# Optimization experiments

Measured on AMD Instinct MI355X. Metric: run time of the kernel, lower is better.

The kernel has to match this reference:

```python
import jax, jax.numpy as jnp
import numpy as np

OUT = 260        # RESIZE_OUTPUT_IMAGES_SHAPE
TH = 0.8         # OD_SCORE_TH
PCT = 1.0        # INTERNAL_PERCENTAGE_IMAGE_TOTAKE
N_BOXES = 10     # loop bound in original call()
TAPS = 6         # lanczos3 support (radius 3 -> 6 taps, antialias=False)


def _lanczos_taps(src, size):
    """src: (OUT,) float sample coords in crop-local space; size: traced int crop size.
    Returns clamped tap indices (OUT,6) and normalized lanczos3 weights (OUT,6)."""
    base = jnp.floor(src).astype(jnp.int32) - 2
    taps = base[:, None] + jnp.arange(TAPS, dtype=jnp.int32)          # (OUT,6)
    d = src[:, None] - taps.astype(src.dtype)
    w = jnp.where(jnp.abs(d) < 3.0, jnp.sinc(d) * jnp.sinc(d / 3.0), 0.0)
    w = w / jnp.sum(w, axis=1, keepdims=True)
    idx = jnp.clip(taps, 0, size - 1)
    return idx, w


def _crop_resize(img, box):
    """img: (H,W,3). box: (4,) normalized [ymin,xmin,ymax,xmax] -> (OUT,OUT,3).
    Matches tf.image.resize lanczos3 (antialias=False): half-pixel centers, clamped edges."""
    H, W = img.shape[0], img.shape[1]
    y0 = (box[0] * H).astype(jnp.int32)
    x0 = (box[1] * W).astype(jnp.int32)
    y1 = (box[2] * H).astype(jnp.int32)
    x1 = (box[3] * W).astype(jnp.int32)
    ch = jnp.maximum(y1 - y0, 1)
    cw = jnp.maximum(x1 - x0, 1)
    o = jnp.arange(OUT, dtype=img.dtype)
    src_h = (o + 0.5) * (ch.astype(img.dtype) / OUT) - 0.5
    src_w = (o + 0.5) * (cw.astype(img.dtype) / OUT) - 0.5
    idx_h, w_h = _lanczos_taps(src_h, ch)
    idx_w, w_w = _lanczos_taps(src_w, cw)
    idx_h = idx_h + y0
    idx_w = idx_w + x0
    # vertical pass: gather 6 row taps per output row, reduce -> (OUT, W, 3)
    rows = jnp.einsum('pa,pawc->pwc', w_h, img[idx_h])
    # horizontal pass: gather 6 col taps per output col, reduce -> (OUT, OUT, 3)
    out = jnp.einsum('qb,pqbc->pqc', w_w, rows[:, idx_w])
    return out


def setup_inputs() -> dict:
    key = jax.random.key(0)
    k1, k2, k3, k4 = jax.random.split(key, 4)
    # scores: first 10 mostly above threshold, rest below
    s_hi = 0.85 + 0.15 * jax.random.uniform(k1, (N_BOXES,), dtype=jnp.float32)
    s_lo = 0.8 * jax.random.uniform(k2, (100 - N_BOXES,), dtype=jnp.float32)
    od_scores = jnp.concatenate([s_hi, s_lo])
    # bboxes (ymin,xmin,ymax,xmax) with guaranteed positive crop sizes
    u = jax.random.uniform(k3, (100, 4), dtype=jnp.float32)
    od_bboxes = jnp.stack([u[:, 0] * 0.45, u[:, 1] * 0.45,
                           0.55 + 0.45 * u[:, 2], 0.55 + 0.45 * u[:, 3]], axis=1)
    image = jax.random.normal(k4, (1, 2048, 2048, 3), dtype=jnp.float32)
    return {"od_scores": od_scores, "od_bboxes": od_bboxes, "image": image}


def reference(od_scores, od_bboxes, image):
    img = image[0]                           # (H,W,3)
    b10 = od_bboxes[:N_BOXES]
    s10 = od_scores[:N_BOXES]
    valid = ((od_scores[0] >= TH) & (s10 >= TH)
             & (b10[:, 1] >= 0.5 - PCT / 2.0)
             & (b10[:, 3] <= 0.5 + PCT / 2.0))
    crops = jax.vmap(lambda b: _crop_resize(img, b))(b10)   # (10,OUT,OUT,3)
    return crops * valid[:, None, None, None].astype(img.dtype)
```

## Files before the change

### kernel.cpp

```cpp
#include <hip/hip_runtime.h>
#include <math.h>

#define OUT 260
#define TAPS 6
#define IMG_H 2048
#define IMG_W 2048
#define ROW_F (IMG_W * 3)
#define NB 10
#define TH 0.8f
#define SEGS 9
#define QB 32
#define LROW 800
#define MAXM 14

__device__ __forceinline__ float sincf(float x) {
    if (x == 0.0f) return 1.0f;
    float px = 3.14159265358979323846f * x;
    return __sinf(px) / px;
}


__global__ __launch_bounds__(320) void tables_kernel(
    const float* __restrict__ scores, const float* __restrict__ boxes,
    float* __restrict__ htab, float* __restrict__ vtab)
{
    const int box = blockIdx.x;
    const float b0 = boxes[box * 4 + 0];
    const float b1 = boxes[box * 4 + 1];
    const float b2 = boxes[box * 4 + 2];
    const float b3 = boxes[box * 4 + 3];

    const int y0 = (int)(b0 * (float)IMG_H);
    const int x0 = (int)(b1 * (float)IMG_W);
    const int y1 = (int)(b2 * (float)IMG_H);
    const int x1 = (int)(b3 * (float)IMG_W);
    const int ch = max(y1 - y0, 1);
    const int cw = max(x1 - x0, 1);

    const bool valid = (scores[0] >= TH) && (scores[box] >= TH)
                    && (b1 >= 0.0f) && (b3 <= 1.0f);
    const float vmask = valid ? 1.0f : 0.0f;

    const int t = threadIdx.x;
    if (t >= OUT) return;

    {
        const float src = ((float)t + 0.5f) * ((float)cw / (float)OUT) - 0.5f;
        const int base = (int)floorf(src) - 2;
        float w[TAPS]; int id[TAPS];
        float s = 0.0f;
        #pragma unroll
        for (int k = 0; k < TAPS; ++k) {
            const float d = src - (float)(base + k);
            const float wv = (fabsf(d) < 3.0f) ? sincf(d) * sincf(d * (1.0f / 3.0f)) : 0.0f;
            w[k] = wv; s += wv;
            int tt = base + k; tt = tt < 0 ? 0 : tt; tt = tt > cw - 1 ? cw - 1 : tt;
            id[k] = (x0 + tt) * 3;
        }
        const float inv = 1.0f / s;
        float* h = htab + ((size_t)(box * OUT + t) << 4);
        int*   hi = (int*)h;
        #pragma unroll
        for (int k = 0; k < TAPS; ++k) { h[k] = w[k] * inv; hi[8 + k] = id[k]; }
        h[6] = 0.0f; h[7] = 0.0f; hi[14] = 0; hi[15] = 0;
    }

    {
        const float src = ((float)t + 0.5f) * ((float)ch / (float)OUT) - 0.5f;
        const int base = (int)floorf(src) - 2;
        float w[TAPS]; int id[TAPS];
        float s = 0.0f;
        #pragma unroll
        for (int k = 0; k < TAPS; ++k) {
            const float d = src - (float)(base + k);
            const float wv = (fabsf(d) < 3.0f) ? sincf(d) * sincf(d * (1.0f / 3.0f)) : 0.0f;
            w[k] = wv; s += wv;
            int tt = base + k; tt = tt < 0 ? 0 : tt; tt = tt > ch - 1 ? ch - 1 : tt;
            id[k] = tt + y0;
        }
        const float inv = vmask / s;
        float* v = vtab + ((size_t)(box * OUT + t) << 4);
        int*   vi = (int*)v;
        #pragma unroll
        for (int k = 0; k < TAPS; ++k) { v[k] = w[k] * inv; vi[8 + k] = id[k]; }
        v[6] = 0.0f; v[7] = 0.0f; vi[14] = base; vi[15] = 0;
    }
}

__global__ __launch_bounds__(64) void crop_resize_pair(
    const float* __restrict__ img,
    const float* __restrict__ htab,
    const float* __restrict__ vtab,
    float* __restrict__ out)
{
    const int seg = blockIdx.x;
    const int py  = blockIdx.y;
    const int box = blockIdx.z;
    const int q0  = seg * QB;
    const int qcount = min(QB, OUT - q0);
    const int p0 = 2 * py;

    const float* v0 = vtab + ((size_t)(box * OUT + p0) << 4);
    const float* v1 = vtab + ((size_t)(box * OUT + p0 + 1) << 4);
    const int* vi0 = (const int*)v0;
    const int* vi1 = (const int*)v1;

    int dlt = vi1[14] - vi0[14];
    dlt = dlt < 0 ? 0 : (dlt > MAXM - TAPS ? MAXM - TAPS : dlt);
    const int m = dlt + TAPS;

    float wa[MAXM], wb[MAXM];
    int   rowi[MAXM];
    #pragma unroll
    for (int j = 0; j < MAXM; ++j) {
        const float wA = (j < TAPS) ? v0[j] : 0.0f;
        const int jb = j - dlt;
        const float wB = (jb >= 0 && jb < TAPS) ? v1[jb] : 0.0f;
        wa[j] = wA; wb[j] = wB;
        rowi[j] = (j < TAPS) ? vi0[8 + j] : vi1[8 + ((jb < 0) ? 0 : (jb > 5 ? 5 : jb))];
    }

    const int* hi_first = (const int*)(htab + ((size_t)(box * OUT + q0) << 4));
    const int* hi_last  = (const int*)(htab + ((size_t)(box * OUT + q0 + qcount - 1) << 4));
    const int start_f = hi_first[8] & ~3;
    const int n_f     = ((hi_last[13] + 3) - start_f + 3) & ~3;

    __shared__ float lds[2 * LROW];

    for (int f = threadIdx.x * 4; f < n_f; f += 64 * 4) {
        float4 a0 = make_float4(0.f, 0.f, 0.f, 0.f);
        float4 a1 = make_float4(0.f, 0.f, 0.f, 0.f);
        #pragma unroll
        for (int j = 0; j < TAPS; ++j) {
            const float4 v = *(const float4*)(img + (size_t)rowi[j] * ROW_F + start_f + f);
            a0.x = fmaf(wa[j], v.x, a0.x); a0.y = fmaf(wa[j], v.y, a0.y);
            a0.z = fmaf(wa[j], v.z, a0.z); a0.w = fmaf(wa[j], v.w, a0.w);
            a1.x = fmaf(wb[j], v.x, a1.x); a1.y = fmaf(wb[j], v.y, a1.y);
            a1.z = fmaf(wb[j], v.z, a1.z); a1.w = fmaf(wb[j], v.w, a1.w);
        }
        for (int j = TAPS; j < m; ++j) {
            const float4 v = *(const float4*)(img + (size_t)rowi[j] * ROW_F + start_f + f);
            a1.x = fmaf(wb[j], v.x, a1.x); a1.y = fmaf(wb[j], v.y, a1.y);
            a1.z = fmaf(wb[j], v.z, a1.z); a1.w = fmaf(wb[j], v.w, a1.w);
        }
        *(float4*)(lds + f) = a0;
        *(float4*)(lds + LROW + f) = a1;
    }
    __syncthreads();

    const int t    = threadIdx.x;
    const int sel  = t >> 5;
    const int qi   = t & 31;
    if (qi < qcount) {
        const int q = q0 + qi;
        const float* h  = htab + ((size_t)(box * OUT + q) << 4);
        const int*   hi = (const int*)h;
        const float* l  = lds + sel * LROW;
        float a0 = 0.0f, a1 = 0.0f, a2 = 0.0f;
        #pragma unroll
        for (int k = 0; k < TAPS; ++k) {
            const float w  = h[k];
            const int   li = hi[8 + k] - start_f;
            a0 = fmaf(w, l[li + 0], a0);
            a1 = fmaf(w, l[li + 1], a1);
            a2 = fmaf(w, l[li + 2], a2);
        }
        const size_t o = (((size_t)box * OUT + (p0 + sel)) * OUT + q) * 3;
        out[o + 0] = a0;
        out[o + 1] = a1;
        out[o + 2] = a2;
    }
}

__global__ __launch_bounds__(256) void crop_resize_fallback(
    const float* __restrict__ scores, const float* __restrict__ boxes,
    const float* __restrict__ img, float* __restrict__ out)
{
    const int p = blockIdx.x, box = blockIdx.y;
    const float b0 = boxes[box*4+0], b1 = boxes[box*4+1];
    const float b2 = boxes[box*4+2], b3 = boxes[box*4+3];
    const int y0 = (int)(b0*(float)IMG_H), x0 = (int)(b1*(float)IMG_W);
    const int y1 = (int)(b2*(float)IMG_H), x1 = (int)(b3*(float)IMG_W);
    const int ch = max(y1-y0,1), cw = max(x1-x0,1);
    const bool valid = (scores[0]>=TH)&&(scores[box]>=TH)&&(b1>=0.0f)&&(b3<=1.0f);
    const float vmask = valid?1.0f:0.0f;
    float wh[TAPS]; int ih[TAPS];
    {
        const float src = ((float)p+0.5f)*((float)ch/(float)OUT)-0.5f;
        const int base = (int)floorf(src)-2;
        float s = 0.0f;
        #pragma unroll
        for (int a = 0; a < TAPS; ++a) {
            const float d = src-(float)(base+a);
            const float w = (fabsf(d)<3.0f)?sincf(d)*sincf(d*(1.0f/3.0f)):0.0f;
            wh[a]=w; s+=w;
            int t=base+a; t=t<0?0:t; t=t>ch-1?ch-1:t; ih[a]=t+y0;
        }
        const float inv = 1.0f/s;
        #pragma unroll
        for (int a = 0; a < TAPS; ++a) wh[a]*=inv;
    }
    const int start_f = (x0*3)&~3;
    const int end_f = (x0+cw)*3;
    const int n_f = end_f-start_f;
    __shared__ float lds[6152];
    {
        const float* r0 = img+(size_t)ih[0]*ROW_F+start_f;
        const float* r1 = img+(size_t)ih[1]*ROW_F+start_f;
        const float* r2 = img+(size_t)ih[2]*ROW_F+start_f;
        const float* r3 = img+(size_t)ih[3]*ROW_F+start_f;
        const float* r4 = img+(size_t)ih[4]*ROW_F+start_f;
        const float* r5 = img+(size_t)ih[5]*ROW_F+start_f;
        for (int f = threadIdx.x*4; f < n_f; f += 256*4) {
            const float4 u0=*(const float4*)(r0+f), u1=*(const float4*)(r1+f);
            const float4 u2=*(const float4*)(r2+f), u3=*(const float4*)(r3+f);
            const float4 u4=*(const float4*)(r4+f), u5=*(const float4*)(r5+f);
            float4 acc;
            acc.x=wh[0]*u0.x+wh[1]*u1.x+wh[2]*u2.x+wh[3]*u3.x+wh[4]*u4.x+wh[5]*u5.x;
            acc.y=wh[0]*u0.y+wh[1]*u1.y+wh[2]*u2.y+wh[3]*u3.y+wh[4]*u4.y+wh[5]*u5.y;
            acc.z=wh[0]*u0.z+wh[1]*u1.z+wh[2]*u2.z+wh[3]*u3.z+wh[4]*u4.z+wh[5]*u5.z;
            acc.w=wh[0]*u0.w+wh[1]*u1.w+wh[2]*u2.w+wh[3]*u3.w+wh[4]*u4.w+wh[5]*u5.w;
            *(float4*)(lds+f)=acc;
        }
    }
    __syncthreads();
    const float wscale = (float)cw/(float)OUT;
    for (int q = threadIdx.x; q < OUT; q += 256) {
        const float src = ((float)q+0.5f)*wscale-0.5f;
        const int basew = (int)floorf(src)-2;
        float ww[TAPS]; float s = 0.0f;
        #pragma unroll
        for (int k = 0; k < TAPS; ++k) {
            const float d = src-(float)(basew+k);
            const float w = (fabsf(d)<3.0f)?sincf(d)*sincf(d*(1.0f/3.0f)):0.0f;
            ww[k]=w; s+=w;
        }
        const float inv = 1.0f/s;
        float a0=0,a1=0,a2=0;
        #pragma unroll
        for (int k = 0; k < TAPS; ++k) {
            int t=basew+k; t=t<0?0:t; t=t>cw-1?cw-1:t;
            const int hb=(x0+t)*3-start_f;
            a0=fmaf(ww[k],lds[hb+0],a0);
            a1=fmaf(ww[k],lds[hb+1],a1);
            a2=fmaf(ww[k],lds[hb+2],a2);
        }
        const float mfac = vmask*inv;
        const size_t o = (((size_t)box*OUT+p)*OUT+q)*3;
        out[o+0]=a0*mfac; out[o+1]=a1*mfac; out[o+2]=a2*mfac;
    }
}

extern "C" void kernel_launch(void* const* d_in, const int* in_sizes, int n_in,
                              void* d_out, int out_size, void* d_ws, size_t ws_size,
                              hipStream_t stream) {
    const float* scores = (const float*)d_in[0];
    const float* boxes  = (const float*)d_in[1];
    const float* img    = (const float*)d_in[2];
    float* out = (float*)d_out;

    const size_t tab_bytes = (size_t)NB * OUT * 16 * sizeof(float);
    if (ws_size < 2 * tab_bytes) {
        crop_resize_fallback<<<dim3(OUT, NB), dim3(256), 0, stream>>>(scores, boxes, img, out);
        return;
    }
    float* htab = (float*)d_ws;
    float* vtab = (float*)((char*)d_ws + tab_bytes);

    tables_kernel<<<dim3(NB), dim3(320), 0, stream>>>(scores, boxes, htab, vtab);
    crop_resize_pair<<<dim3(SEGS, OUT / 2, NB), dim3(64), 0, stream>>>(img, htab, vtab, out);
}
```

Before: 119.2 us.

## Compute four output rows per block sharing a union of image row loads

Replaces the two-rows-per-block vertical pass with a block that handles a group of four output rows, loading the union of their source image rows once and accumulating into four register accumulators per float4 column chunk. Column segments widen to 48 outputs, so fewer blocks re-read overlapping image columns, and the per-row weight/index tables are staged in shared memory. This cuts redundant global reads of image rows at the cost of many more accumulator registers (80 floats) and a larger LDS footprint, which may lower occupancy, and fewer total blocks.

```diff
diff --git a/kernel.cpp b/kernel.cpp
--- a/kernel.cpp
+++ b/kernel.cpp
@@ -8,10 +8,12 @@
 #define ROW_F (IMG_W * 3)
 #define NB 10
 #define TH 0.8f
-#define SEGS 9
-#define QB 32
-#define LROW 800
-#define MAXM 14
+#define SEGS 6
+#define QB 48
+#define G 4
+#define LROW 1152
+#define MAXM 32
+#define NF 5
 
 __device__ __forceinline__ float sincf(float x) {
     if (x == 0.0f) return 1.0f;
@@ -87,37 +89,63 @@
     }
 }
 
-__global__ __launch_bounds__(64) void crop_resize_pair(
+__global__ __launch_bounds__(64) void crop_resize_pg(
     const float* __restrict__ img,
+    const float* __restrict__ boxes,
     const float* __restrict__ htab,
     const float* __restrict__ vtab,
     float* __restrict__ out)
 {
     const int seg = blockIdx.x;
-    const int py  = blockIdx.y;
+    const int pg  = blockIdx.y;
     const int box = blockIdx.z;
     const int q0  = seg * QB;
     const int qcount = min(QB, OUT - q0);
-    const int p0 = 2 * py;
-
-    const float* v0 = vtab + ((size_t)(box * OUT + p0) << 4);
-    const float* v1 = vtab + ((size_t)(box * OUT + p0 + 1) << 4);
-    const int* vi0 = (const int*)v0;
-    const int* vi1 = (const int*)v1;
-
-    int dlt = vi1[14] - vi0[14];
-    dlt = dlt < 0 ? 0 : (dlt > MAXM - TAPS ? MAXM - TAPS : dlt);
-    const int m = dlt + TAPS;
-
-    float wa[MAXM], wb[MAXM];
-    int   rowi[MAXM];
-    #pragma unroll
-    for (int j = 0; j < MAXM; ++j) {
-        const float wA = (j < TAPS) ? v0[j] : 0.0f;
-        const int jb = j - dlt;
-        const float wB = (jb >= 0 && jb < TAPS) ? v1[jb] : 0.0f;
-        wa[j] = wA; wb[j] = wB;
-        rowi[j] = (j < TAPS) ? vi0[8 + j] : vi1[8 + ((jb < 0) ? 0 : (jb > 5 ? 5 : jb))];
+    const int p0 = pg * G;
+    const int tid = threadIdx.x;
+
+    __shared__ float ldsrow[G * LROW];
+    __shared__ float wlds[G * MAXM];
+    __shared__ int   rowlds[MAXM];
+
+    const float b0 = boxes[box * 4 + 0];
+    const float b2 = boxes[box * 4 + 2];
+    const int y0 = (int)(b0 * (float)IMG_H);
+    const int y1 = (int)(b2 * (float)IMG_H);
+    const int ch = max(y1 - y0, 1);
+
+    const int base0 = ((const int*)(vtab + ((size_t)(box * OUT + p0) << 4)))[14];
+    const int baseL = ((const int*)(vtab + ((size_t)(box * OUT + p0 + G - 1) << 4)))[14];
+    int m = baseL - base0 + TAPS;
+    m = m < TAPS ? TAPS : (m > MAXM ? MAXM : m);
+
+    for (int idx = tid; idx < G * MAXM; idx += 64) {
+        const int g = idx >> 5;
+        const int j = idx & (MAXM - 1);
+        const float* vg = vtab + ((size_t)(box * OUT + p0 + g) << 4);
+        const int dg = ((const int*)vg)[14] - base0;
+        const int k = j - dg;
+        wlds[idx] = (k >= 0 && k < TAPS) ? vg[k] : 0.0f;
+    }
+    if (tid < MAXM) {
+        int r = base0 + tid;
+        r = r < 0 ? 0 : (r > ch - 1 ? ch - 1 : r);
+        rowlds[tid] = r + y0;
+    }
+
+    const int q = q0 + tid;
+    const bool qact = (tid < qcount);
+    float hw0 = 0, hw1 = 0, hw2 = 0, hw3 = 0, hw4 = 0, hw5 = 0;
+    int li0 = 0, li1 = 0, li2 = 0, li3 = 0, li4 = 0, li5 = 0;
+    if (qact) {
+        const float* h = htab + ((size_t)(box * OUT + q) << 4);
+        const int*  hi = (const int*)h;
+        const float4 w01 = *(const float4*)(h);
+        const float4 w23 = *(const float4*)(h + 4);
+        hw0 = w01.x; hw1 = w01.y; hw2 = w01.z; hw3 = w01.w;
+        hw4 = w23.x; hw5 = w23.y;
+        li0 = hi[8]; li1 = hi[9]; li2 = hi[10];
+        li3 = hi[11]; li4 = hi[12]; li5 = hi[13];
     }
 
     const int* hi_first = (const int*)(htab + ((size_t)(box * OUT + q0) << 4));
@@ -125,50 +153,67 @@
     const int start_f = hi_first[8] & ~3;
     const int n_f     = ((hi_last[13] + 3) - start_f + 3) & ~3;
 
-    __shared__ float lds[2 * LROW];
-
-    for (int f = threadIdx.x * 4; f < n_f; f += 64 * 4) {
-        float4 a0 = make_float4(0.f, 0.f, 0.f, 0.f);
-        float4 a1 = make_float4(0.f, 0.f, 0.f, 0.f);
-        #pragma unroll
-        for (int j = 0; j < TAPS; ++j) {
-            const float4 v = *(const float4*)(img + (size_t)rowi[j] * ROW_F + start_f + f);
-            a0.x = fmaf(wa[j], v.x, a0.x); a0.y = fmaf(wa[j], v.y, a0.y);
-            a0.z = fmaf(wa[j], v.z, a0.z); a0.w = fmaf(wa[j], v.w, a0.w);
-            a1.x = fmaf(wb[j], v.x, a1.x); a1.y = fmaf(wb[j], v.y, a1.y);
-            a1.z = fmaf(wb[j], v.z, a1.z); a1.w = fmaf(wb[j], v.w, a1.w);
-        }
-        for (int j = TAPS; j < m; ++j) {
-            const float4 v = *(const float4*)(img + (size_t)rowi[j] * ROW_F + start_f + f);
-            a1.x = fmaf(wb[j], v.x, a1.x); a1.y = fmaf(wb[j], v.y, a1.y);
-            a1.z = fmaf(wb[j], v.z, a1.z); a1.w = fmaf(wb[j], v.w, a1.w);
-        }
-        *(float4*)(lds + f) = a0;
-        *(float4*)(lds + LROW + f) = a1;
-    }
     __syncthreads();
 
-    const int t    = threadIdx.x;
-    const int sel  = t >> 5;
-    const int qi   = t & 31;
-    if (qi < qcount) {
-        const int q = q0 + qi;
-        const float* h  = htab + ((size_t)(box * OUT + q) << 4);
-        const int*   hi = (const int*)h;
-        const float* l  = lds + sel * LROW;
-        float a0 = 0.0f, a1 = 0.0f, a2 = 0.0f;
-        #pragma unroll
-        for (int k = 0; k < TAPS; ++k) {
-            const float w  = h[k];
-            const int   li = hi[8 + k] - start_f;
-            a0 = fmaf(w, l[li + 0], a0);
-            a1 = fmaf(w, l[li + 1], a1);
-            a2 = fmaf(w, l[li + 2], a2);
-        }
-        const size_t o = (((size_t)box * OUT + (p0 + sel)) * OUT + q) * 3;
-        out[o + 0] = a0;
-        out[o + 1] = a1;
-        out[o + 2] = a2;
+    float4 acc[NF][G];
+    #pragma unroll
+    for (int i = 0; i < NF; ++i)
+        #pragma unroll
+        for (int g = 0; g < G; ++g)
+            acc[i][g] = make_float4(0.f, 0.f, 0.f, 0.f);
+
+    for (int j = 0; j < m; ++j) {
+        const int row = rowlds[j];
+        const float w0 = wlds[0 * MAXM + j];
+        const float w1 = wlds[1 * MAXM + j];
+        const float w2 = wlds[2 * MAXM + j];
+        const float w3 = wlds[3 * MAXM + j];
+        const float* rp = img + (size_t)row * ROW_F + start_f;
+        #pragma unroll
+        for (int i = 0; i < NF; ++i) {
+            const int f = tid * 4 + i * 256;
+            if (f < n_f) {
+                const float4 v = *(const float4*)(rp + f);
+                acc[i][0].x = fmaf(w0, v.x, acc[i][0].x); acc[i][0].y = fmaf(w0, v.y, acc[i][0].y);
+                acc[i][0].z = fmaf(w0, v.z, acc[i][0].z); acc[i][0].w = fmaf(w0, v.w, acc[i][0].w);
+                acc[i][1].x = fmaf(w1, v.x, acc[i][1].x); acc[i][1].y = fmaf(w1, v.y, acc[i][1].y);
+                acc[i][1].z = fmaf(w1, v.z, acc[i][1].z); acc[i][1].w = fmaf(w1, v.w, acc[i][1].w);
+                acc[i][2].x = fmaf(w2, v.x, acc[i][2].x); acc[i][2].y = fmaf(w2, v.y, acc[i][2].y);
+                acc[i][2].z = fmaf(w2, v.z, acc[i][2].z); acc[i][2].w = fmaf(w2, v.w, acc[i][2].w);
+                acc[i][3].x = fmaf(w3, v.x, acc[i][3].x); acc[i][3].y = fmaf(w3, v.y, acc[i][3].y);
+                acc[i][3].z = fmaf(w3, v.z, acc[i][3].z); acc[i][3].w = fmaf(w3, v.w, acc[i][3].w);
+            }
+        }
+    }
+    #pragma unroll
+    for (int i = 0; i < NF; ++i) {
+        const int f = tid * 4 + i * 256;
+        if (f < n_f) {
+            #pragma unroll
+            for (int g = 0; g < G; ++g)
+                *(float4*)(ldsrow + g * LROW + f) = acc[i][g];
+        }
+    }
+    __syncthreads();
+
+    if (qact) {
+        const int i0 = li0 - start_f, i1 = li1 - start_f, i2 = li2 - start_f;
+        const int i3 = li3 - start_f, i4 = li4 - start_f, i5 = li5 - start_f;
+        #pragma unroll
+        for (int g = 0; g < G; ++g) {
+            const float* l = ldsrow + g * LROW;
+            float a0, a1, a2;
+            a0 = hw0 * l[i0 + 0]; a1 = hw0 * l[i0 + 1]; a2 = hw0 * l[i0 + 2];
+            a0 = fmaf(hw1, l[i1 + 0], a0); a1 = fmaf(hw1, l[i1 + 1], a1); a2 = fmaf(hw1, l[i1 + 2], a2);
+            a0 = fmaf(hw2, l[i2 + 0], a0); a1 = fmaf(hw2, l[i2 + 1], a1); a2 = fmaf(hw2, l[i2 + 2], a2);
+            a0 = fmaf(hw3, l[i3 + 0], a0); a1 = fmaf(hw3, l[i3 + 1], a1); a2 = fmaf(hw3, l[i3 + 2], a2);
+            a0 = fmaf(hw4, l[i4 + 0], a0); a1 = fmaf(hw4, l[i4 + 1], a1); a2 = fmaf(hw4, l[i4 + 2], a2);
+            a0 = fmaf(hw5, l[i5 + 0], a0); a1 = fmaf(hw5, l[i5 + 1], a1); a2 = fmaf(hw5, l[i5 + 2], a2);
+            const size_t o = (((size_t)box * OUT + (p0 + g)) * OUT + q) * 3;
+            out[o + 0] = a0;
+            out[o + 1] = a1;
+            out[o + 2] = a2;
+        }
     }
 }
 
@@ -268,5 +313,5 @@
     float* vtab = (float*)((char*)d_ws + tab_bytes);
 
     tables_kernel<<<dim3(NB), dim3(320), 0, stream>>>(scores, boxes, htab, vtab);
-    crop_resize_pair<<<dim3(SEGS, OUT / 2, NB), dim3(64), 0, stream>>>(img, htab, vtab, out);
-}
+    crop_resize_pg<<<dim3(SEGS, OUT / G, NB), dim3(64), 0, stream>>>(img, boxes, htab, vtab, out);
+}
```

New measurement: 156.1 us. 1.31x slower.
